# Kernel optimization log

Hardware: AMD Instinct MI355X
Metric: run time of the kernel (lower is better)

## Reference

```python
import jax, jax.numpy as jnp
import numpy as np

TEMPERATURE = 0.07


def setup_inputs() -> dict:
    key = jax.random.key(0)
    k1, k2 = jax.random.split(key)
    embeddings = jax.random.normal(k1, (8192, 256), dtype=jnp.float32)
    labels = jax.random.randint(k2, (8192,), 0, 1024, dtype=jnp.int64)
    return {"embeddings": embeddings, "labels": labels}


def reference(embeddings, labels):
    b = embeddings.shape[0]
    # L2 normalize rows (torch F.normalize uses eps=1e-12 clamp on the norm)
    norm = jnp.linalg.norm(embeddings, axis=1, keepdims=True)
    en = embeddings / jnp.maximum(norm, 1e-12)
    # [B, B] similarity scaled by temperature
    sim = jnp.matmul(en, en.T) / TEMPERATURE
    # log-softmax over rows (denominator includes the diagonal, as in the original)
    logp = jax.nn.log_softmax(sim, axis=1)
    # positive mask: same label, excluding self
    mask = (labels[:, None] == labels[None, :]) & ~jnp.eye(b, dtype=bool)
    pos_mask = mask.astype(logp.dtype)
    pos_count = pos_mask.sum(axis=1)
    pos_sum = -jnp.sum(logp * pos_mask, axis=1)
    pos_loss = jnp.where(pos_count > 0, pos_sum / jnp.maximum(pos_count, 1.0), 0.0)
    return pos_loss.mean()
```

## Files before the change

kernel.cpp:

```cpp
#include <hip/hip_runtime.h>
#include <hip/hip_bf16.h>

#define B_N 8192
#define D_K 256
#define BM  256
#define BN  32
#define JSPLIT 16
#define JSPAN (B_N / JSPLIT)
#define NTILE (JSPAN / BN)
#define NCLS 1024
#define INVT 14.285714285714286f
#define C1   20.60992907f

typedef __bf16 bf16x8 __attribute__((ext_vector_type(8)));
typedef float  f32x16 __attribute__((ext_vector_type(16)));
typedef float  f32x4  __attribute__((ext_vector_type(4)));

#define AS1 __attribute__((address_space(1)))
#define AS3 __attribute__((address_space(3)))

__device__ __forceinline__ unsigned short f32_to_bf16_rne(float f) {
    unsigned int u = __float_as_uint(f);
    unsigned int r = (u + 0x7FFFu + ((u >> 16) & 1u)) >> 16;
    return (unsigned short)r;
}
__device__ __forceinline__ float bf16_to_f32(unsigned short u) {
    return __uint_as_float(((unsigned int)u) << 16);
}

__global__ void zero_kernel(float* __restrict__ out, int* __restrict__ hist) {
    int g = blockIdx.x * 256 + threadIdx.x;
    if (g < NCLS) hist[g] = 0;
    if (g == 0) out[0] = 0.0f;
}

__global__ void norm_kernel(const float* __restrict__ emb,
                            const int* __restrict__ labels,
                            unsigned short* __restrict__ en,
                            int* __restrict__ hist) {
    const int t = threadIdx.x;
    const int w = t >> 6, l = t & 63;
    const int row = blockIdx.x * 4 + w;
    f32x4 x = *reinterpret_cast<const f32x4*>(emb + (size_t)row * D_K + l * 4);
    float ss = x[0]*x[0] + x[1]*x[1] + x[2]*x[2] + x[3]*x[3];
    #pragma unroll
    for (int m = 1; m < 64; m <<= 1) ss += __shfl_xor(ss, m, 64);
    float sc = 1.0f / fmaxf(sqrtf(ss), 1e-12f);
    ushort4 o;
    o.x = f32_to_bf16_rne(x[0] * sc); o.y = f32_to_bf16_rne(x[1] * sc);
    o.z = f32_to_bf16_rne(x[2] * sc); o.w = f32_to_bf16_rne(x[3] * sc);
    *reinterpret_cast<ushort4*>(en + (size_t)row * D_K + l * 4) = o;
    if (l == 0) atomicAdd(&hist[labels[row]], 1);
}

__launch_bounds__(256, 2)
__global__ void loss_kernel(const unsigned short* __restrict__ en,
                            const int* __restrict__ labels,
                            float* __restrict__ s_part,
                            float* __restrict__ ps_part) {
    __shared__ __align__(16) unsigned short Bls[2][BN * D_K];
    __shared__ __align__(16) int Lab_s[JSPAN];

    const int t  = threadIdx.x;
    const int l  = t & 63;
    const int w  = t >> 6;
    const int ir = l & 31;
    const int h  = l >> 5;

    const int b      = blockIdx.x;
    const int xcd    = b & 7;
    const int local  = b >> 3;
    const int itile  = xcd * 4 + (local & 3);
    const int jsplit = local >> 2;
    const int ibase  = itile * BM;
    const int j0     = jsplit * JSPAN;

    bf16x8 bi0[16], bi1[16];
    {
        const unsigned short* ap0 =
            en + (size_t)(ibase + w * 64 + ir) * D_K + h * 8;
        const unsigned short* ap1 = ap0 + 32 * D_K;
        #pragma unroll
        for (int ks = 0; ks < 16; ++ks) {
            bi0[ks] = *reinterpret_cast<const bf16x8*>(ap0 + ks * 16);
            bi1[ks] = *reinterpret_cast<const bf16x8*>(ap1 + ks * 16);
        }
    }
    const int li0 = labels[ibase + w * 64 + ir];
    const int li1 = labels[ibase + w * 64 + 32 + ir];

    const int srcm = (t & 31) ^ ((t >> 5) & 7);
    const unsigned short* gb =
        en + (size_t)(j0 + (t >> 5)) * D_K + srcm * 8;
    const char* abase0 = (const char*)Bls[0] + (size_t)ir * 512;
    const char* abase1 = (const char*)Bls[1] + (size_t)ir * 512;
    const int xr = (ir & 7) << 4;

    float sA0 = 0.f, sA1 = 0.f, sB0 = 0.f, sB1 = 0.f;
    float pA0 = 0.f, pA1 = 0.f, pB0 = 0.f, pB1 = 0.f;

#define STAGE(bufp, itv)                                                     \
    {                                                                        \
        const unsigned short* gsrc = gb + (size_t)(itv) * (BN * D_K);        \
        char* ldst = (char*)(bufp) + t * 16;                                 \
        _Pragma("unroll")                                                    \
        for (int rd = 0; rd < 4; ++rd)                                       \
            __builtin_amdgcn_global_load_lds(                                \
                (const AS1 void*)(gsrc + rd * 2048),                         \
                (AS3 void*)(ldst + rd * 4096), 16, 0, 0);                    \
    }

#define TILE_COMPUTE(arow_b, itv)                                            \
    {                                                                        \
        int ljv[16];                                                         \
        {                                                                    \
            const int lb = (itv) * BN + h * 4;                               \
            *(int4*)&ljv[0]  = *(const int4*)&Lab_s[lb];                     \
            *(int4*)&ljv[4]  = *(const int4*)&Lab_s[lb + 8];                 \
            *(int4*)&ljv[8]  = *(const int4*)&Lab_s[lb + 16];                \
            *(int4*)&ljv[12] = *(const int4*)&Lab_s[lb + 24];                \
        }                                                                    \
        f32x16 a0, a1;                                                       \
        _Pragma("unroll")                                                    \
        for (int q = 0; q < 16; ++q) { a0[q] = 0.0f; a1[q] = 0.0f; }         \
        __builtin_amdgcn_s_setprio(1);                                       \
        _Pragma("unroll")                                                    \
        for (int ks = 0; ks < 16; ++ks) {                                    \
            const bf16x8 af = *reinterpret_cast<const bf16x8*>(              \
                (arow_b) + ((((ks << 1) | h) << 4) ^ xr));                   \
            a0 = __builtin_amdgcn_mfma_f32_32x32x16_bf16(af, bi0[ks], a0,    \
                                                         0, 0, 0);           \
            a1 = __builtin_amdgcn_mfma_f32_32x32x16_bf16(af, bi1[ks], a1,    \
                                                         0, 0, 0);           \
        }                                                                    \
        __builtin_amdgcn_s_setprio(0);                                       \
        _Pragma("unroll")                                                    \
        for (int q = 0; q < 16; ++q) {                                       \
            float d0 = a0[q], d1 = a1[q];                                    \
            float e0 = __builtin_amdgcn_exp2f(fmaf(d0, C1, -C1));            \
            float e1 = __builtin_amdgcn_exp2f(fmaf(d1, C1, -C1));            \
            if (q & 1) {                                                     \
                sA1 += e0; pA1 += (ljv[q] == li0) ? d0 : 0.0f;               \
                sB1 += e1; pB1 += (ljv[q] == li1) ? d1 : 0.0f;               \
            } else {                                                         \
                sA0 += e0; pA0 += (ljv[q] == li0) ? d0 : 0.0f;               \
                sB0 += e1; pB0 += (ljv[q] == li1) ? d1 : 0.0f;               \
            }                                                                \
        }                                                                    \
    }

    STAGE(Bls[0], 0);
    Lab_s[t]       = labels[j0 + t];
    Lab_s[t + 256] = labels[j0 + t + 256];
    __syncthreads();

    for (int it = 0; it < NTILE; it += 2) {
        if (it + 1 < NTILE) STAGE(Bls[1], it + 1);
        TILE_COMPUTE(abase0, it);
        asm volatile("s_waitcnt vmcnt(0)");
        __syncthreads();
        if (it + 2 < NTILE) STAGE(Bls[0], it + 2);
        TILE_COMPUTE(abase1, it + 1);
        asm volatile("s_waitcnt vmcnt(0)");
        __syncthreads();
    }
#undef STAGE
#undef TILE_COMPUTE

    float sA = sA0 + sA1, pA = pA0 + pA1;
    float sB = sB0 + sB1, pB = pB0 + pB1;
    sA += __shfl_xor(sA, 32, 64);  pA += __shfl_xor(pA, 32, 64);
    sB += __shfl_xor(sB, 32, 64);  pB += __shfl_xor(pB, 32, 64);
    if (h == 0) {
        const size_t base = (size_t)jsplit * B_N + ibase + w * 64 + ir;
        s_part[base]       = sA;
        ps_part[base]      = pA;
        s_part[base + 32]  = sB;
        ps_part[base + 32] = pB;
    }
}

__global__ void final_kernel(const unsigned short* __restrict__ en,
                             const int* __restrict__ labels,
                             const float* __restrict__ s_part,
                             const float* __restrict__ ps_part,
                             const int* __restrict__ hist,
                             float* __restrict__ out) {
    const int t = threadIdx.x, w = t >> 6, l = t & 63;
    const int i = blockIdx.x * 4 + w;
    ushort4 eu = *reinterpret_cast<const ushort4*>(en + (size_t)i * D_K + l * 4);
    float e0 = bf16_to_f32(eu.x), e1 = bf16_to_f32(eu.y),
          e2 = bf16_to_f32(eu.z), e3 = bf16_to_f32(eu.w);
    float self = e0 * e0 + e1 * e1 + e2 * e2 + e3 * e3;
    #pragma unroll
    for (int m = 1; m < 64; m <<= 1) self += __shfl_xor(self, m, 64);
    __shared__ float part[4];
    if (l == 0) {
        float s = 0.f, ps = 0.f;
        #pragma unroll
        for (int k = 0; k < JSPLIT; ++k) {
            s  += s_part[k * B_N + i];
            ps += ps_part[k * B_N + i];
        }
        ps -= self;
        int pc = hist[labels[i]] - 1;
        float loss = (pc > 0) ? (INVT + logf(s)) - ps * INVT / (float)pc : 0.0f;
        part[w] = loss;
    }
    __syncthreads();
    if (t == 0)
        atomicAdd(out, (part[0] + part[1] + part[2] + part[3]) * (1.0f / B_N));
}

extern "C" void kernel_launch(void* const* d_in, const int* in_sizes, int n_in,
                              void* d_out, int out_size, void* d_ws, size_t ws_size,
                              hipStream_t stream) {
    const float* emb    = (const float*)d_in[0];
    const int*   labels = (const int*)d_in[1];
    float*       out    = (float*)d_out;

    unsigned short* en = (unsigned short*)d_ws;
    float* s_part  = (float*)((char*)d_ws + (size_t)B_N * D_K * 2);
    float* ps_part = s_part + JSPLIT * B_N;
    int*   hist    = (int*)(ps_part + JSPLIT * B_N);

    hipLaunchKernelGGL(zero_kernel, dim3(4), dim3(256), 0, stream, out, hist);
    hipLaunchKernelGGL(norm_kernel, dim3(B_N / 4), dim3(256), 0, stream,
                       emb, labels, en, hist);
    hipLaunchKernelGGL(loss_kernel, dim3((B_N / BM) * JSPLIT), dim3(256), 0,
                       stream, en, labels, s_part, ps_part);
    hipLaunchKernelGGL(final_kernel, dim3(B_N / 4), dim3(256), 0, stream,
                       en, labels, s_part, ps_part, hist, out);
}
```

Before: 130.9 us.

## Deepen B-tile pipeline to four buffers and slim final reduction kernel

The loss kernel's double-buffered LDS staging becomes a 4-slot ring with three tiles in flight. It waits on partial vmcnt counts and uses one barrier per tile, where before it drained all loads and synced twice per pair. The self-dot term is now computed in the norm kernel and stored, so the final kernel runs one thread per row with coalesced partial reads instead of one wave per row. The zero kernel is replaced by memset calls. LDS use doubles to 64KB per block, which may reduce occupancy, and the partial vmcnt waits depend on exact counts of outstanding loads.

```diff
diff --git a/kernel.cpp b/kernel.cpp
--- a/kernel.cpp
+++ b/kernel.cpp
@@ -28,16 +28,11 @@
     return __uint_as_float(((unsigned int)u) << 16);
 }
 
-__global__ void zero_kernel(float* __restrict__ out, int* __restrict__ hist) {
-    int g = blockIdx.x * 256 + threadIdx.x;
-    if (g < NCLS) hist[g] = 0;
-    if (g == 0) out[0] = 0.0f;
-}
-
 __global__ void norm_kernel(const float* __restrict__ emb,
                             const int* __restrict__ labels,
                             unsigned short* __restrict__ en,
-                            int* __restrict__ hist) {
+                            int* __restrict__ hist,
+                            float* __restrict__ self_arr) {
     const int t = threadIdx.x;
     const int w = t >> 6, l = t & 63;
     const int row = blockIdx.x * 4 + w;
@@ -50,7 +45,15 @@
     o.x = f32_to_bf16_rne(x[0] * sc); o.y = f32_to_bf16_rne(x[1] * sc);
     o.z = f32_to_bf16_rne(x[2] * sc); o.w = f32_to_bf16_rne(x[3] * sc);
     *reinterpret_cast<ushort4*>(en + (size_t)row * D_K + l * 4) = o;
-    if (l == 0) atomicAdd(&hist[labels[row]], 1);
+    float y0 = bf16_to_f32(o.x), y1 = bf16_to_f32(o.y),
+          y2 = bf16_to_f32(o.z), y3 = bf16_to_f32(o.w);
+    float s2 = y0*y0 + y1*y1 + y2*y2 + y3*y3;
+    #pragma unroll
+    for (int m = 1; m < 64; m <<= 1) s2 += __shfl_xor(s2, m, 64);
+    if (l == 0) {
+        self_arr[row] = s2;
+        atomicAdd(&hist[labels[row]], 1);
+    }
 }
 
 __launch_bounds__(256, 2)
@@ -58,7 +61,7 @@
                             const int* __restrict__ labels,
                             float* __restrict__ s_part,
                             float* __restrict__ ps_part) {
-    __shared__ __align__(16) unsigned short Bls[2][BN * D_K];
+    __shared__ __align__(16) unsigned short Bls[4 * BN * D_K];
     __shared__ __align__(16) int Lab_s[JSPAN];
 
     const int t  = threadIdx.x;
@@ -92,17 +95,15 @@
     const int srcm = (t & 31) ^ ((t >> 5) & 7);
     const unsigned short* gb =
         en + (size_t)(j0 + (t >> 5)) * D_K + srcm * 8;
-    const char* abase0 = (const char*)Bls[0] + (size_t)ir * 512;
-    const char* abase1 = (const char*)Bls[1] + (size_t)ir * 512;
     const int xr = (ir & 7) << 4;
 
     float sA0 = 0.f, sA1 = 0.f, sB0 = 0.f, sB1 = 0.f;
     float pA0 = 0.f, pA1 = 0.f, pB0 = 0.f, pB1 = 0.f;
 
-#define STAGE(bufp, itv)                                                     \
+#define STAGE(bufi, itv)                                                     \
     {                                                                        \
         const unsigned short* gsrc = gb + (size_t)(itv) * (BN * D_K);        \
-        char* ldst = (char*)(bufp) + t * 16;                                 \
+        char* ldst = (char*)Bls + (size_t)(bufi) * 16384 + t * 16;           \
         _Pragma("unroll")                                                    \
         for (int rd = 0; rd < 4; ++rd)                                       \
             __builtin_amdgcn_global_load_lds(                                \
@@ -110,8 +111,10 @@
                 (AS3 void*)(ldst + rd * 4096), 16, 0, 0);                    \
     }
 
-#define TILE_COMPUTE(arow_b, itv)                                            \
+#define TILE_COMPUTE(bufi, itv)                                              \
     {                                                                        \
+        const char* arow =                                                   \
+            (const char*)Bls + (size_t)(bufi) * 16384 + (size_t)ir * 512;    \
         int ljv[16];                                                         \
         {                                                                    \
             const int lb = (itv) * BN + h * 4;                               \
@@ -127,7 +130,7 @@
         _Pragma("unroll")                                                    \
         for (int ks = 0; ks < 16; ++ks) {                                    \
             const bf16x8 af = *reinterpret_cast<const bf16x8*>(              \
-                (arow_b) + ((((ks << 1) | h) << 4) ^ xr));                   \
+                arow + ((((ks << 1) | h) << 4) ^ xr));                       \
             a0 = __builtin_amdgcn_mfma_f32_32x32x16_bf16(af, bi0[ks], a0,    \
                                                          0, 0, 0);           \
             a1 = __builtin_amdgcn_mfma_f32_32x32x16_bf16(af, bi1[ks], a1,    \
@@ -149,20 +152,23 @@
         }                                                                    \
     }
 
-    STAGE(Bls[0], 0);
     Lab_s[t]       = labels[j0 + t];
     Lab_s[t + 256] = labels[j0 + t + 256];
-    __syncthreads();
-
-    for (int it = 0; it < NTILE; it += 2) {
-        if (it + 1 < NTILE) STAGE(Bls[1], it + 1);
-        TILE_COMPUTE(abase0, it);
-        asm volatile("s_waitcnt vmcnt(0)");
-        __syncthreads();
-        if (it + 2 < NTILE) STAGE(Bls[0], it + 2);
-        TILE_COMPUTE(abase1, it + 1);
-        asm volatile("s_waitcnt vmcnt(0)");
-        __syncthreads();
+    STAGE(0, 0);
+    STAGE(1, 1);
+    STAGE(2, 2);
+    asm volatile("s_waitcnt lgkmcnt(0)" ::: "memory");
+
+    for (int it = 0; it < NTILE; ++it) {
+        if (it + 2 < NTILE)
+            asm volatile("s_waitcnt vmcnt(8)" ::: "memory");
+        else if (it + 1 < NTILE)
+            asm volatile("s_waitcnt vmcnt(4)" ::: "memory");
+        else
+            asm volatile("s_waitcnt vmcnt(0)" ::: "memory");
+        __builtin_amdgcn_s_barrier();
+        if (it + 3 < NTILE) STAGE((it + 3) & 3, it + 3);
+        TILE_COMPUTE(it & 3, it);
     }
 #undef STAGE
 #undef TILE_COMPUTE
@@ -180,33 +186,27 @@
     }
 }
 
-__global__ void final_kernel(const unsigned short* __restrict__ en,
-                             const int* __restrict__ labels,
+__global__ void final_kernel(const int* __restrict__ labels,
                              const float* __restrict__ s_part,
                              const float* __restrict__ ps_part,
+                             const float* __restrict__ self_arr,
                              const int* __restrict__ hist,
                              float* __restrict__ out) {
-    const int t = threadIdx.x, w = t >> 6, l = t & 63;
-    const int i = blockIdx.x * 4 + w;
-    ushort4 eu = *reinterpret_cast<const ushort4*>(en + (size_t)i * D_K + l * 4);
-    float e0 = bf16_to_f32(eu.x), e1 = bf16_to_f32(eu.y),
-          e2 = bf16_to_f32(eu.z), e3 = bf16_to_f32(eu.w);
-    float self = e0 * e0 + e1 * e1 + e2 * e2 + e3 * e3;
-    #pragma unroll
-    for (int m = 1; m < 64; m <<= 1) self += __shfl_xor(self, m, 64);
+    const int t = threadIdx.x;
+    const int i = blockIdx.x * 256 + t;
+    float s = 0.f, ps = 0.f;
+    #pragma unroll
+    for (int k = 0; k < JSPLIT; ++k) {
+        s  += s_part[(size_t)k * B_N + i];
+        ps += ps_part[(size_t)k * B_N + i];
+    }
+    ps -= self_arr[i];
+    int pc = hist[labels[i]] - 1;
+    float loss = (pc > 0) ? (INVT + logf(s)) - ps * INVT / (float)pc : 0.0f;
+    #pragma unroll
+    for (int m = 1; m < 64; m <<= 1) loss += __shfl_xor(loss, m, 64);
     __shared__ float part[4];
-    if (l == 0) {
-        float s = 0.f, ps = 0.f;
-        #pragma unroll
-        for (int k = 0; k < JSPLIT; ++k) {
-            s  += s_part[k * B_N + i];
-            ps += ps_part[k * B_N + i];
-        }
-        ps -= self;
-        int pc = hist[labels[i]] - 1;
-        float loss = (pc > 0) ? (INVT + logf(s)) - ps * INVT / (float)pc : 0.0f;
-        part[w] = loss;
-    }
+    if ((t & 63) == 0) part[t >> 6] = loss;
     __syncthreads();
     if (t == 0)
         atomicAdd(out, (part[0] + part[1] + part[2] + part[3]) * (1.0f / B_N));
@@ -223,12 +223,14 @@
     float* s_part  = (float*)((char*)d_ws + (size_t)B_N * D_K * 2);
     float* ps_part = s_part + JSPLIT * B_N;
     int*   hist    = (int*)(ps_part + JSPLIT * B_N);
-
-    hipLaunchKernelGGL(zero_kernel, dim3(4), dim3(256), 0, stream, out, hist);
+    float* self_arr = (float*)(hist + NCLS);
+
+    hipMemsetAsync(out, 0, sizeof(float) * out_size, stream);
+    hipMemsetAsync(hist, 0, sizeof(int) * NCLS, stream);
     hipLaunchKernelGGL(norm_kernel, dim3(B_N / 4), dim3(256), 0, stream,
-                       emb, labels, en, hist);
+                       emb, labels, en, hist, self_arr);
     hipLaunchKernelGGL(loss_kernel, dim3((B_N / BM) * JSPLIT), dim3(256), 0,
                        stream, en, labels, s_part, ps_part);
-    hipLaunchKernelGGL(final_kernel, dim3(B_N / 4), dim3(256), 0, stream,
-                       en, labels, s_part, ps_part, hist, out);
-}
+    hipLaunchKernelGGL(final_kernel, dim3(B_N / 256), dim3(256), 0, stream,
+                       labels, s_part, ps_part, self_arr, hist, out);
+}
```

New measurement: 110.0 us. -16.0%, faster.
